# Kernel tuning notes

Hardware: AMD Instinct MI355X
Metric: run time of the kernel (lower is better)

The kernel has to match this reference:

```python
import jax, jax.numpy as jnp
import numpy as np

INPUT_DIM = 1024
HIDDEN_DIM = 1024
NUM_HEADS = 16
HEAD_DIM = HIDDEN_DIM // NUM_HEADS


def setup_inputs() -> dict:
    key = jax.random.key(0)
    ks = jax.random.split(key, 11)
    B, S = 2, 2048
    s_in = 1.0 / np.sqrt(INPUT_DIM)
    s_hid = 1.0 / np.sqrt(HIDDEN_DIM)
    return {
        "query": jax.random.normal(ks[0], (B, S, INPUT_DIM), jnp.float32),
        "key": jax.random.normal(ks[1], (B, S, INPUT_DIM), jnp.float32),
        "value": jax.random.normal(ks[2], (B, S, INPUT_DIM), jnp.float32),
        "Wq": jax.random.normal(ks[3], (INPUT_DIM, HIDDEN_DIM), jnp.float32) * s_in,
        "bq": jnp.zeros((HIDDEN_DIM,), jnp.float32),
        "Wk": jax.random.normal(ks[4], (INPUT_DIM, HEAD_DIM), jnp.float32) * s_in,
        "bk": jnp.zeros((HEAD_DIM,), jnp.float32),
        "Wv": jax.random.normal(ks[5], (INPUT_DIM, HEAD_DIM), jnp.float32) * s_in,
        "bv": jnp.zeros((HEAD_DIM,), jnp.float32),
        "Wo": jax.random.normal(ks[6], (HIDDEN_DIM, INPUT_DIM), jnp.float32) * s_hid,
        "bo": jnp.zeros((INPUT_DIM,), jnp.float32),
    }


def reference(query, key, value, Wq, bq, Wk, bk, Wv, bv, Wo, bo):
    B, S, _ = query.shape
    # projections
    q = query @ Wq + bq                       # [B,S,H*D]
    k = key @ Wk + bk                         # [B,S,D]  (single shared head)
    v = value @ Wv + bv                       # [B,S,D]
    q = q.reshape(B, S, NUM_HEADS, HEAD_DIM)  # [B,S,H,D]
    # MQA scores: shared K broadcast over query heads
    scores = jnp.einsum('bqhd,bkd->bhqk', q, k) / np.sqrt(HIDDEN_DIM)
    attn = jax.nn.softmax(scores, axis=-1)    # [B,H,Q,K]
    out = jnp.einsum('bhqk,bkd->bqhd', attn, v)  # [B,Q,H,D]
    out = out.reshape(B, S, HIDDEN_DIM)
    return out @ Wo + bo
```

## Files before the change

### kernel.cpp

```cpp
#include <hip/hip_runtime.h>


typedef unsigned int   u32;
typedef unsigned short u16;
typedef union { float4 v; float f[4]; } f4u;
typedef __attribute__((ext_vector_type(8)))  short frag16;
typedef __attribute__((ext_vector_type(4)))  float f32x4;
typedef __attribute__((ext_vector_type(16))) float f32x16;
typedef union { frag16 v; u32 w[4]; u16 e[8]; } bf8u;

static __device__ __forceinline__ u16 f2bf(float x) {
  union { float f; u32 u; } v; v.f = x;
  u32 r = v.u + 0x7fff + ((v.u >> 16) & 1);
  return (u16)(r >> 16);
}

static __device__ __forceinline__ u32 cvt_pk_bf16(float lo, float hi) {
  u32 r;
  asm("v_cvt_pk_bf16_f32 %0, %1, %2" : "=v"(r) : "v"(lo), "v"(hi));
  return r;
}

static __device__ void tcvt_tile(const float* __restrict__ src,
                                 u16* __restrict__ dst,
                                 int C, int ldT, int rt, int ct,
                                 float (*t)[65]) {
  const int r0 = rt * 64, c0 = ct * 64;
  const int tr  = threadIdx.x >> 4;
  const int tc4 = (threadIdx.x & 15) * 4;
#pragma unroll
  for (int i = 0; i < 4; ++i) {
    f4u v; v.v = *(const float4*)(src + (size_t)(r0 + tr + i * 16) * C + c0 + tc4);
    t[tr + i * 16][tc4 + 0] = v.f[0];
    t[tr + i * 16][tc4 + 1] = v.f[1];
    t[tr + i * 16][tc4 + 2] = v.f[2];
    t[tr + i * 16][tc4 + 3] = v.f[3];
  }
  __syncthreads();
#pragma unroll
  for (int i = 0; i < 4; ++i) {
    const int oc = tr + i * 16;
    ushort4 o;
    o.x = f2bf(t[tc4 + 0][oc]);
    o.y = f2bf(t[tc4 + 1][oc]);
    o.z = f2bf(t[tc4 + 2][oc]);
    o.w = f2bf(t[tc4 + 3][oc]);
    *(ushort4*)(dst + (size_t)(c0 + oc) * ldT + r0 + tc4) = o;
  }
}

__global__ __launch_bounds__(256)
void prep_w(const float* __restrict__ Wq, const float* __restrict__ Wo,
            const float* __restrict__ Wk, const float* __restrict__ Wv,
            u16* __restrict__ wq_t, u16* __restrict__ wo_t,
            u16* __restrict__ wk_t, u16* __restrict__ wv_t) {
  __shared__ float t[64][65];
  const int bid = blockIdx.x;
  if (bid < 256)      tcvt_tile(Wq, wq_t, 1024, 1024, bid >> 4, bid & 15, t);
  else if (bid < 512) tcvt_tile(Wo, wo_t, 1024, 1024, (bid - 256) >> 4, (bid - 256) & 15, t);
  else if (bid < 528) tcvt_tile(Wk, wk_t, 64, 1024, bid - 512, 0, t);
  else                tcvt_tile(Wv, wv_t, 64, 1024, bid - 528, 0, t);
}

#define GP 72
template <bool A_FP32>
static __device__ void gemm64(const float* __restrict__ Af32,
                              const u16* __restrict__ Abf,
                              const u16* __restrict__ Bt,
                              const float* __restrict__ bias,
                              void* __restrict__ Cout, int out_mode,
                              float oscale,
                              int row0, int col0, int N, int K, int ldT,
                              u16* As, u16* Bs) {
  const int tid  = threadIdx.x;
  const int lane = tid & 63;
  const int quad = lane >> 4, l15 = lane & 15;
  const int w = tid >> 6, wy = w >> 1, wx = w & 1;

  f32x4 acc[2][2];
#pragma unroll
  for (int i = 0; i < 2; ++i)
#pragma unroll
    for (int j = 0; j < 2; ++j) {
      acc[i][j][0] = 0.f; acc[i][j][1] = 0.f;
      acc[i][j][2] = 0.f; acc[i][j][3] = 0.f;
    }

  const int r = tid >> 2, c16 = (tid & 3) * 16;

  for (int k0 = 0; k0 < K; k0 += 64) {
    frag16 a0, a1;
    if (A_FP32) {
      const float* ap = Af32 + (size_t)(row0 + r) * K + k0 + c16;
      f4u x0, x1, x2, x3;
      x0.v = *(const float4*)(ap);
      x1.v = *(const float4*)(ap + 4);
      x2.v = *(const float4*)(ap + 8);
      x3.v = *(const float4*)(ap + 12);
      bf8u t0, t1;
      t0.w[0] = cvt_pk_bf16(x0.f[0], x0.f[1]);
      t0.w[1] = cvt_pk_bf16(x0.f[2], x0.f[3]);
      t0.w[2] = cvt_pk_bf16(x1.f[0], x1.f[1]);
      t0.w[3] = cvt_pk_bf16(x1.f[2], x1.f[3]);
      t1.w[0] = cvt_pk_bf16(x2.f[0], x2.f[1]);
      t1.w[1] = cvt_pk_bf16(x2.f[2], x2.f[3]);
      t1.w[2] = cvt_pk_bf16(x3.f[0], x3.f[1]);
      t1.w[3] = cvt_pk_bf16(x3.f[2], x3.f[3]);
      a0 = t0.v; a1 = t1.v;
    } else {
      const u16* ap = Abf + (size_t)(row0 + r) * K + k0 + c16;
      a0 = *(const frag16*)(ap);
      a1 = *(const frag16*)(ap + 8);
    }
    const u16* bp = Bt + (size_t)(col0 + r) * K + k0 + c16;
    const frag16 b0 = *(const frag16*)(bp);
    const frag16 b1 = *(const frag16*)(bp + 8);
    __syncthreads();
    *(frag16*)(&As[r * GP + c16])     = a0;
    *(frag16*)(&As[r * GP + c16 + 8]) = a1;
    *(frag16*)(&Bs[r * GP + c16])     = b0;
    *(frag16*)(&Bs[r * GP + c16 + 8]) = b1;
    __syncthreads();
#pragma unroll
    for (int ks = 0; ks < 2; ++ks) {
      frag16 af[2], bf[2];
#pragma unroll
      for (int i = 0; i < 2; ++i)
        af[i] = *(const frag16*)(&As[(wy * 32 + i * 16 + l15) * GP + ks * 32 + quad * 8]);
#pragma unroll
      for (int j = 0; j < 2; ++j)
        bf[j] = *(const frag16*)(&Bs[(wx * 32 + j * 16 + l15) * GP + ks * 32 + quad * 8]);
#pragma unroll
      for (int i = 0; i < 2; ++i)
#pragma unroll
        for (int j = 0; j < 2; ++j)
          acc[i][j] = __builtin_amdgcn_mfma_f32_16x16x32_bf16(af[i], bf[j], acc[i][j], 0, 0, 0);
    }
  }

  float bj[2];
#pragma unroll
  for (int j = 0; j < 2; ++j)
    bj[j] = bias[col0 + wx * 32 + j * 16 + l15];

#pragma unroll
  for (int i = 0; i < 2; ++i) {
#pragma unroll
    for (int rr = 0; rr < 4; ++rr) {
      const size_t row = row0 + wy * 32 + i * 16 + quad * 4 + rr;
#pragma unroll
      for (int j = 0; j < 2; ++j) {
        const float v = (acc[i][j][rr] + bj[j]) * oscale;
        const int col = col0 + wx * 32 + j * 16 + l15;
        if (out_mode == 0)      ((float*)Cout)[row * N + col] = v;
        else if (out_mode == 1) ((u16*)Cout)[row * N + col] = f2bf(v);
        else                    ((u16*)Cout)[(size_t)col * ldT + row] = f2bf(v);
      }
    }
  }
}

#define C2_SCALE 0.045084220027780106f

__global__ __launch_bounds__(256, 4)
void proj(const float* __restrict__ query, const float* __restrict__ key,
          const float* __restrict__ value,
          const u16* __restrict__ wq_t, const u16* __restrict__ wk_t,
          const u16* __restrict__ wv_t,
          const float* __restrict__ bq, const float* __restrict__ bk,
          const float* __restrict__ bv,
          u16* __restrict__ q_bf, u16* __restrict__ k_bf,
          u16* __restrict__ vt_bf, int M, int K) {
  __shared__ __align__(16) u16 As[64 * GP];
  __shared__ __align__(16) u16 Bs[64 * GP];
  const int bid = blockIdx.x;
  if (bid < 64)
    gemm64<true>(key, nullptr, wk_t, bk, k_bf, 1, 1.0f, bid * 64, 0, 64, K, 0, As, Bs);
  else if (bid < 128)
    gemm64<true>(value, nullptr, wv_t, bv, vt_bf, 2, 1.0f, (bid - 64) * 64, 0, 64, K, M, As, Bs);
  else {
    const int q = bid - 128;
    gemm64<true>(query, nullptr, wq_t, bq, q_bf, 1, C2_SCALE,
                 (q >> 4) * 64, (q & 15) * 64, 1024, K, 0, As, Bs);
  }
}

__global__ __launch_bounds__(256, 4)
void out_proj(const u16* __restrict__ ao, const u16* __restrict__ wo_t,
              const float* __restrict__ bo, float* __restrict__ out,
              int M, int K) {
  __shared__ __align__(16) u16 As[64 * GP];
  __shared__ __align__(16) u16 Bs[64 * GP];
  gemm64<false>(nullptr, ao, wo_t, bo, out, 0, 1.0f,
                blockIdx.y * 64, blockIdx.x * 64, 1024, K, 0, As, Bs);
}

#define APITCH 72

__global__ __launch_bounds__(256)
void mqa_flash_mfma(const u16* __restrict__ Qb,
                    const u16* __restrict__ Kb,
                    const u16* __restrict__ Vt,
                    u16* __restrict__ O) {
  const int S = 2048, HID = 1024, D = 64, BS = 4096;
  __shared__ u16 Ks[64 * APITCH];
  __shared__ u16 Vs[64 * APITCH];
  __shared__ u16 Ps[64 * APITCH];
  __shared__ float red[2][64];

  const int tid  = threadIdx.x;
  const int lane = tid & 63;
  const int w    = tid >> 6;
  const int l31  = lane & 31;
  const int hh   = lane >> 5;
  const int kh   = w & 1;
  const int qh   = w >> 1;
  const int qb = blockIdx.x, h = blockIdx.y, b = blockIdx.z;

  const u16* qrow = Qb + (size_t)(b * S + qb * 64 + qh * 32 + l31) * HID + h * D;
  frag16 qf[4];
#pragma unroll
  for (int ks = 0; ks < 4; ++ks)
    qf[ks] = *(const frag16*)(qrow + ks * 16 + hh * 8);

  f32x16 zero16;
#pragma unroll
  for (int r = 0; r < 16; ++r) zero16[r] = 0.f;

  f32x16 o_acc;
#pragma unroll
  for (int r = 0; r < 16; ++r) o_acc[r] = 0.f;
  float l_lane = 0.f;

  for (int kc = 0; kc < S; kc += 64) {
    __syncthreads();
    {
      const u16* ksrc = Kb + (size_t)(b * S + kc) * D;
      const u16* vsrc = Vt + (size_t)(b * S + kc);
#pragma unroll
      for (int i = 0; i < 2; ++i) {
        const int c = tid + i * 256;
        const int r = c >> 3, col = (c & 7) * 8;
        *(frag16*)(&Ks[r * APITCH + col]) = *(const frag16*)(ksrc + r * D + col);
        *(frag16*)(&Vs[r * APITCH + col]) = *(const frag16*)(vsrc + (size_t)r * BS + col);
      }
    }
    __syncthreads();

    f32x16 sa;
#pragma unroll
    for (int ks = 0; ks < 4; ++ks) {
      const frag16 kf = *(const frag16*)(&Ks[(kh * 32 + l31) * APITCH + ks * 16 + hh * 8]);
      sa = __builtin_amdgcn_mfma_f32_32x32x16_bf16(kf, qf[ks], ks ? sa : zero16, 0, 0, 0);
    }

    const int qrow_l = qh * 32 + l31;
    u16* prow = &Ps[qrow_l * APITCH + kh * 32];
#pragma unroll
    for (int g = 0; g < 4; ++g) {
      const float p0 = __builtin_amdgcn_exp2f(sa[g * 4 + 0]);
      const float p1 = __builtin_amdgcn_exp2f(sa[g * 4 + 1]);
      const float p2 = __builtin_amdgcn_exp2f(sa[g * 4 + 2]);
      const float p3 = __builtin_amdgcn_exp2f(sa[g * 4 + 3]);
      l_lane += (p0 + p1) + (p2 + p3);
      uint2 pk;
      pk.x = cvt_pk_bf16(p0, p1);
      pk.y = cvt_pk_bf16(p2, p3);
      *(uint2*)(&prow[g * 8 + hh * 4]) = pk;
    }
    __syncthreads();

#pragma unroll
    for (int ks = 0; ks < 4; ++ks) {
      const frag16 pf = *(const frag16*)(&Ps[(qh * 32 + l31) * APITCH + ks * 16 + hh * 8]);
      const frag16 vf = *(const frag16*)(&Vs[(kh * 32 + l31) * APITCH + ks * 16 + hh * 8]);
      o_acc = __builtin_amdgcn_mfma_f32_32x32x16_bf16(pf, vf, o_acc, 0, 0, 0);
    }
  }

  l_lane += __shfl_xor(l_lane, 32);
  __syncthreads();
  if (lane < 32) red[kh][qh * 32 + l31] = l_lane;
  __syncthreads();

#pragma unroll
  for (int r = 0; r < 16; ++r) {
    const int q_local = qh * 32 + (r & 3) + 8 * (r >> 2) + 4 * hh;
    const float li = 1.f / (red[0][q_local] + red[1][q_local]);
    u16* orow = O + (size_t)(b * S + qb * 64 + q_local) * HID + h * D;
    orow[kh * 32 + l31] = f2bf(o_acc[r] * li);
  }
}

extern "C" void kernel_launch(void* const* d_in, const int* in_sizes, int n_in,
                              void* d_out, int out_size, void* d_ws, size_t ws_size,
                              hipStream_t stream) {
  const float* query = (const float*)d_in[0];
  const float* key   = (const float*)d_in[1];
  const float* value = (const float*)d_in[2];
  const float* Wq    = (const float*)d_in[3];
  const float* bq    = (const float*)d_in[4];
  const float* Wk    = (const float*)d_in[5];
  const float* bk    = (const float*)d_in[6];
  const float* Wv    = (const float*)d_in[7];
  const float* bv    = (const float*)d_in[8];
  const float* Wo    = (const float*)d_in[9];
  const float* bo    = (const float*)d_in[10];
  float* out = (float*)d_out;

  const int B = 2, S = 2048, IN = 1024, HID = 1024, H = 16, D = 64;
  const int M = B * S;
  const size_t MB = 1024 * 1024;

  char* ws = (char*)d_ws;
  u16* q_bf  = (u16*)ws;
  u16* ao_bf = (u16*)(ws + 8 * MB);
  u16* k_bf  = (u16*)(ws + 16 * MB);
  u16* vt_bf = (u16*)(ws + 16 * MB + 512 * 1024);
  u16* wq_t  = (u16*)(ws + 17 * MB);
  u16* wo_t  = (u16*)(ws + 19 * MB);
  u16* wk_t  = (u16*)(ws + 21 * MB);
  u16* wv_t  = (u16*)(ws + 21 * MB + 128 * 1024);

  dim3 blk(256);
  prep_w<<<dim3(544), blk, 0, stream>>>(Wq, Wo, Wk, Wv, wq_t, wo_t, wk_t, wv_t);
  proj<<<dim3(1152), blk, 0, stream>>>(query, key, value, wq_t, wk_t, wv_t,
                                       bq, bk, bv, q_bf, k_bf, vt_bf, M, IN);
  mqa_flash_mfma<<<dim3(S / 64, H, B), blk, 0, stream>>>(q_bf, k_bf, vt_bf, ao_bf);
  out_proj<<<dim3(HID / 64, M / 64), blk, 0, stream>>>(ao_bf, wo_t, bo, out, M, HID);
}
```

Baseline: 217.3 us.

## Prefetch next K/V tile into registers and drop a barrier in MQA attention

The attention loop now issues global loads for the next 64-key K and V tiles into registers at the start of each iteration. It writes them to shared memory only after the PV MFMAs finish, so global latency overlaps the score, softmax and PV work. V fragments are read from shared memory early into registers, which lets one __syncthreads per iteration be removed. A min-blocks-per-CU hint of 4 is also added to the launch bounds, which may limit registers per thread and risks spills given the extra prefetch and V-fragment registers.

```diff
diff --git a/kernel.cpp b/kernel.cpp
--- a/kernel.cpp
+++ b/kernel.cpp
@@ -197,7 +197,7 @@
 
 #define APITCH 72
 
-__global__ __launch_bounds__(256)
+__global__ __launch_bounds__(256, 4)
 void mqa_flash_mfma(const u16* __restrict__ Qb,
                     const u16* __restrict__ Kb,
                     const u16* __restrict__ Vt,
@@ -217,6 +217,9 @@
   const int qh   = w >> 1;
   const int qb = blockIdx.x, h = blockIdx.y, b = blockIdx.z;
 
+  const int sr = tid >> 3;
+  const int sc = (tid & 7) * 8;
+
   const u16* qrow = Qb + (size_t)(b * S + qb * 64 + qh * 32 + l31) * HID + h * D;
   frag16 qf[4];
 #pragma unroll
@@ -232,20 +235,30 @@
   for (int r = 0; r < 16; ++r) o_acc[r] = 0.f;
   float l_lane = 0.f;
 
+  const u16* kbase = Kb + (size_t)(b * S) * D;
+  const u16* vbase = Vt + (size_t)(b * S);
+
+  frag16 pk0 = *(const frag16*)(kbase + (size_t)sr * D + sc);
+  frag16 pk1 = *(const frag16*)(kbase + (size_t)(sr + 32) * D + sc);
+  frag16 pv0 = *(const frag16*)(vbase + (size_t)sr * BS + sc);
+  frag16 pv1 = *(const frag16*)(vbase + (size_t)(sr + 32) * BS + sc);
+  *(frag16*)(&Ks[sr * APITCH + sc])        = pk0;
+  *(frag16*)(&Ks[(sr + 32) * APITCH + sc]) = pk1;
+  *(frag16*)(&Vs[sr * APITCH + sc])        = pv0;
+  *(frag16*)(&Vs[(sr + 32) * APITCH + sc]) = pv1;
+  __syncthreads();
+
   for (int kc = 0; kc < S; kc += 64) {
-    __syncthreads();
-    {
-      const u16* ksrc = Kb + (size_t)(b * S + kc) * D;
-      const u16* vsrc = Vt + (size_t)(b * S + kc);
-#pragma unroll
-      for (int i = 0; i < 2; ++i) {
-        const int c = tid + i * 256;
-        const int r = c >> 3, col = (c & 7) * 8;
-        *(frag16*)(&Ks[r * APITCH + col]) = *(const frag16*)(ksrc + r * D + col);
-        *(frag16*)(&Vs[r * APITCH + col]) = *(const frag16*)(vsrc + (size_t)r * BS + col);
-      }
-    }
-    __syncthreads();
+    const int nc = (kc + 64 < S) ? kc + 64 : kc;
+    pk0 = *(const frag16*)(kbase + (size_t)(nc + sr) * D + sc);
+    pk1 = *(const frag16*)(kbase + (size_t)(nc + sr + 32) * D + sc);
+    pv0 = *(const frag16*)(vbase + (size_t)sr * BS + nc + sc);
+    pv1 = *(const frag16*)(vbase + (size_t)(sr + 32) * BS + nc + sc);
+
+    frag16 vf[4];
+#pragma unroll
+    for (int ks = 0; ks < 4; ++ks)
+      vf[ks] = *(const frag16*)(&Vs[(kh * 32 + l31) * APITCH + ks * 16 + hh * 8]);
 
     f32x16 sa;
 #pragma unroll
@@ -273,9 +286,14 @@
 #pragma unroll
     for (int ks = 0; ks < 4; ++ks) {
       const frag16 pf = *(const frag16*)(&Ps[(qh * 32 + l31) * APITCH + ks * 16 + hh * 8]);
-      const frag16 vf = *(const frag16*)(&Vs[(kh * 32 + l31) * APITCH + ks * 16 + hh * 8]);
-      o_acc = __builtin_amdgcn_mfma_f32_32x32x16_bf16(pf, vf, o_acc, 0, 0, 0);
-    }
+      o_acc = __builtin_amdgcn_mfma_f32_32x32x16_bf16(pf, vf[ks], o_acc, 0, 0, 0);
+    }
+
+    *(frag16*)(&Ks[sr * APITCH + sc])        = pk0;
+    *(frag16*)(&Ks[(sr + 32) * APITCH + sc]) = pk1;
+    *(frag16*)(&Vs[sr * APITCH + sc])        = pv0;
+    *(frag16*)(&Vs[(sr + 32) * APITCH + sc]) = pv1;
+    __syncthreads();
   }
 
   l_lane += __shfl_xor(l_lane, 32);
```

After: 216.5 us. No clear change (-0.4%).
